# Kernel tuning notes

Hardware: AMD Instinct MI355X
Metric: run time of the kernel (lower is better)

## Reference

```python
import jax, jax.numpy as jnp
import numpy as np

INP_DIM = 1024
PROJ_DIM = 1024
SEQ = 2048
BATCH = 4

def setup_inputs() -> dict:
    key = jax.random.key(0)
    k1, k2, k3, k4 = jax.random.split(key, 4)
    inputs = jax.random.normal(k1, (BATCH, SEQ, INP_DIM), dtype=jnp.float32)
    # nn.Linear weights stored as (out, in); we keep them that way and transpose in matmul
    Wq = jax.random.normal(k2, (PROJ_DIM, INP_DIM), dtype=jnp.float32) * (1.0 / np.sqrt(INP_DIM))
    Wk = jax.random.normal(k3, (PROJ_DIM, INP_DIM), dtype=jnp.float32) * (1.0 / np.sqrt(INP_DIM))
    Wv = jax.random.normal(k4, (PROJ_DIM, INP_DIM), dtype=jnp.float32) * (1.0 / np.sqrt(INP_DIM))
    return {"inputs": inputs, "Wq": Wq, "Wk": Wk, "Wv": Wv}

def reference(inputs, Wq, Wk, Wv):
    # QKV projections: x @ W.T (nn.Linear convention)
    Q = jnp.einsum('bsd,pd->bsp', inputs, Wq)
    K = jnp.einsum('bsd,pd->bsp', inputs, Wk)
    V = jnp.einsum('bsd,pd->bsp', inputs, Wv)
    scores = jnp.einsum('bqp,bkp->bqk', Q, K)  # [B, S, S]
    n = inputs.shape[1]
    causal = jnp.tril(jnp.ones((n, n), dtype=bool))  # True = keep
    scores = jnp.where(causal, scores, -jnp.inf)
    weights = jax.nn.softmax(scores / jnp.sqrt(jnp.float32(Q.shape[-1])), axis=-1)
    # dropout rate = 0.0 -> identity
    Z = jnp.einsum('bqk,bkp->bqp', weights, V)
    return Z
```

## Files before the change

kernel.cpp:

```cpp
#include <hip/hip_runtime.h>
#include <stdint.h>

#define SEQ   2048
#define DIM   1024
#define BATCH 4

typedef _Float16 f16;
typedef __attribute__((ext_vector_type(8))) _Float16 f16x8;
typedef __attribute__((ext_vector_type(4))) _Float16 f16x4;
typedef __attribute__((ext_vector_type(4))) float   f32x4;

typedef void __attribute__((address_space(1))) vg_t;
typedef void __attribute__((address_space(3))) vl_t;

__device__ __forceinline__ void gld16(const void* g, void* l) {
  __builtin_amdgcn_global_load_lds((vg_t*)g, (vl_t*)l, 16, 0, 0);
}

__global__ __launch_bounds__(256) void cvt_all(const float* __restrict__ x,
                                               const float* __restrict__ wq,
                                               const float* __restrict__ wk,
                                               const float* __restrict__ wv,
                                               f16* __restrict__ xb,
                                               f16* __restrict__ wh) {
  const int bx = blockIdx.x;
  const float* in; f16* out; int base;
  if (bx < 8192)       { in = x;  out = xb;             base = bx; }
  else if (bx < 9216)  { in = wq; out = wh;             base = bx - 8192; }
  else if (bx < 10240) { in = wk; out = wh + (1 << 20); base = bx - 9216; }
  else                 { in = wv; out = wh + (2 << 20); base = bx - 10240; }
  const long i = ((long)base * 256 + threadIdx.x) * 4;
  float4 v = *(const float4*)(in + i);
  f16x4 o = { (f16)v.x, (f16)v.y, (f16)v.z, (f16)v.w };
  *(f16x4*)(out + i) = o;
}

template <int MODE, int CAUSAL, int BK>
__global__ __launch_bounds__(256) void gemm_bt(const f16* __restrict__ A, int lda, long aOffZ,
                                               const f16* __restrict__ B, int ldb, long bOffZ,
                                               void* __restrict__ Cv, int ldc, long cOffZ,
                                               int K) {
  constexpr int CH  = BK / 8;
  constexpr int RPL = 64 / CH;
  constexpr int NL  = 32 / RPL;
  __shared__ __align__(16) f16 lA[128 * BK];
  __shared__ __align__(16) f16 lB[128 * BK];

  const int tid  = threadIdx.x;
  const int wave = tid >> 6;
  const int lane = tid & 63;
  const int m0 = blockIdx.x * 128;
  const int n0 = blockIdx.y * 128;
  const int z  = blockIdx.z;

  if (CAUSAL == 1 && n0 >= m0 + 128) return;
  const int Keff = (CAUSAL == 2) ? (m0 + 128) : K;

  const f16* Ab = A + (long)z * aOffZ + (long)m0 * lda;
  const f16* Bb = B + (long)z * bOffZ + (long)n0 * ldb;

  const int wm = (wave & 1) * 64;
  const int wn = (wave >> 1) * 64;

  f32x4 acc[4][4] = {};

  const int srow = lane / CH;
  const int sj   = lane % CH;
  const int fr   = lane & 15;
  const int fq   = lane >> 4;

  for (int kt = 0; kt < Keff; kt += BK) {
    __syncthreads();
#pragma unroll
    for (int j = 0; j < NL; ++j) {
      const int rgrp = j * 4 + wave;
      const int row  = rgrp * RPL + srow;
      const int gch  = sj ^ (row & (CH - 1));
      gld16(Ab + (long)row * lda + kt + gch * 8, (void*)(lA + rgrp * 512 + lane * 8));
      gld16(Bb + (long)row * ldb + kt + gch * 8, (void*)(lB + rgrp * 512 + lane * 8));
    }
    __syncthreads();

#pragma unroll
    for (int kk = 0; kk < BK; kk += 32) {
      f16x8 af[4], bf[4];
#pragma unroll
      for (int i = 0; i < 4; ++i) {
        const int arow = wm + i * 16 + fr;
        const int ach  = (kk / 8 + fq) ^ (arow & (CH - 1));
        af[i] = *(const f16x8*)(lA + arow * BK + ach * 8);
        const int brow = wn + i * 16 + fr;
        const int bch  = (kk / 8 + fq) ^ (brow & (CH - 1));
        bf[i] = *(const f16x8*)(lB + brow * BK + bch * 8);
      }
#pragma unroll
      for (int mi = 0; mi < 4; ++mi)
#pragma unroll
        for (int ni = 0; ni < 4; ++ni)
          acc[mi][ni] = __builtin_amdgcn_mfma_f32_16x16x32_f16(af[mi], bf[ni], acc[mi][ni], 0, 0, 0);
    }
  }

#pragma unroll
  for (int mi = 0; mi < 4; ++mi) {
    const int row = m0 + wm + mi * 16 + fq * 4;
#pragma unroll
    for (int ni = 0; ni < 4; ++ni) {
      const int col = n0 + wn + ni * 16 + fr;
      if constexpr (MODE == 0) {
        float* C = (float*)Cv + (long)z * cOffZ;
#pragma unroll
        for (int r = 0; r < 4; ++r) C[(long)(row + r) * ldc + col] = acc[mi][ni][r];
      } else if constexpr (MODE == 1) {
        f16* C = (f16*)Cv + (long)z * cOffZ;
#pragma unroll
        for (int r = 0; r < 4; ++r) C[(long)(row + r) * ldc + col] = (f16)acc[mi][ni][r];
      } else if constexpr (MODE == 2) {
        f16* C = (f16*)Cv + (long)z * cOffZ;
        f16x4 o = { (f16)acc[mi][ni][0], (f16)acc[mi][ni][1],
                    (f16)acc[mi][ni][2], (f16)acc[mi][ni][3] };
        *(f16x4*)(C + (long)col * ldc + row) = o;
      } else {
        f16* Qh  = (f16*)Cv;
        f16* Kh  = Qh + (size_t)8 * 1024 * 1024;
        f16* VTb = Kh + (size_t)8 * 1024 * 1024;
        if (col < 1024) {
#pragma unroll
          for (int r = 0; r < 4; ++r) Qh[(long)(row + r) * DIM + col] = (f16)acc[mi][ni][r];
        } else if (col < 2048) {
#pragma unroll
          for (int r = 0; r < 4; ++r) Kh[(long)(row + r) * DIM + (col - 1024)] = (f16)acc[mi][ni][r];
        } else {
          f16x4 o = { (f16)acc[mi][ni][0], (f16)acc[mi][ni][1],
                      (f16)acc[mi][ni][2], (f16)acc[mi][ni][3] };
          *(f16x4*)(VTb + (long)(col - 2048) * (BATCH * SEQ) + row) = o;
        }
      }
    }
  }
}

__global__ __launch_bounds__(256) void softmax_causal(f16* S) {
  const int q = blockIdx.x, b = blockIdx.y;
  f16* row = S + ((long)b * SEQ + q) * SEQ;
  const int tid = threadIdx.x;
  const int lane = tid & 63, wave = tid >> 6;
  const int nvalid = q + 1;

  f16x8 vv = *(const f16x8*)(row + tid * 8);
  float v[8];
  float m = -3.0e38f;
#pragma unroll
  for (int i = 0; i < 8; ++i) {
    const int k = tid * 8 + i;
    v[i] = (k < nvalid) ? (float)vv[i] * 0.03125f : -3.0e38f;
    m = fmaxf(m, v[i]);
  }
#pragma unroll
  for (int off = 32; off; off >>= 1) m = fmaxf(m, __shfl_xor(m, off));
  __shared__ float redm[4], reds[4];
  if (lane == 0) redm[wave] = m;
  __syncthreads();
  m = fmaxf(fmaxf(redm[0], redm[1]), fmaxf(redm[2], redm[3]));

  float s = 0.f;
#pragma unroll
  for (int i = 0; i < 8; ++i) {
    const float p = (v[i] > -1.0e37f) ? __expf(v[i] - m) : 0.f;
    v[i] = p;
    s += p;
  }
#pragma unroll
  for (int off = 32; off; off >>= 1) s += __shfl_xor(s, off);
  if (lane == 0) reds[wave] = s;
  __syncthreads();
  s = reds[0] + reds[1] + reds[2] + reds[3];
  const float inv = 1.f / s;
  f16x8 o;
#pragma unroll
  for (int i = 0; i < 8; ++i) o[i] = (f16)(v[i] * inv);
  *(f16x8*)(row + tid * 8) = o;
}

extern "C" void kernel_launch(void* const* d_in, const int* in_sizes, int n_in,
                              void* d_out, int out_size, void* d_ws, size_t ws_size,
                              hipStream_t stream) {
  const float* x  = (const float*)d_in[0];
  const float* Wq = (const float*)d_in[1];
  const float* Wk = (const float*)d_in[2];
  const float* Wv = (const float*)d_in[3];
  float* out = (float*)d_out;

  if (ws_size < (size_t)51 * 1024 * 1024 * 2) return;

  f16* xb = (f16*)d_ws;
  f16* Wh = xb + (size_t)8 * 1024 * 1024;
  f16* Qh = Wh + (size_t)3 * 1024 * 1024;
  f16* Kh = Qh + (size_t)8 * 1024 * 1024;
  f16* VT = Kh + (size_t)8 * 1024 * 1024;
  f16* Sc = VT + (size_t)8 * 1024 * 1024;

  const long QOFF = (long)SEQ * DIM;
  const long SOFF = (long)SEQ * SEQ;

  cvt_all<<<11264, 256, 0, stream>>>(x, Wq, Wk, Wv, xb, Wh);

  gemm_bt<3, 0, 64><<<dim3(64, 24, 1), 256, 0, stream>>>(xb, DIM, 0, Wh, DIM, 0, Qh, 0, 0, DIM);

  gemm_bt<1, 1, 128><<<dim3(16, 16, 4), 256, 0, stream>>>(Qh, DIM, QOFF, Kh, DIM, QOFF,
                                                          Sc, SEQ, SOFF, DIM);

  softmax_causal<<<dim3(SEQ, BATCH), 256, 0, stream>>>(Sc);

  gemm_bt<0, 2, 128><<<dim3(16, 8, 4), 256, 0, stream>>>(Sc, SEQ, SOFF,
                                                         VT, BATCH * SEQ, SEQ,
                                                         out, DIM, (long)SEQ * DIM, SEQ);
}
```

Before: 244.4 us.

## Double-buffer LDS tiles in GEMM to overlap global loads with MFMA

Replaces the single-buffered shared-memory K loop with a two-stage ping-pong buffer so the next K tile's async global-to-LDS loads are issued before computing the current tile. BK is fixed at 64 for all GEMMs, so the two GEMMs that used BK=128 now run more, smaller iterations. LDS use per block stays at 64 KB. The goal is to hide global memory latency behind MFMA work, at the cost of fewer K elements per barrier interval for those GEMMs.

New measurement: 255.0 us. 1.04x slower.

```diff
diff --git a/kernel.cpp b/kernel.cpp
--- a/kernel.cpp
+++ b/kernel.cpp
@@ -35,16 +35,14 @@
   *(f16x4*)(out + i) = o;
 }
 
-template <int MODE, int CAUSAL, int BK>
+template <int MODE, int CAUSAL>
 __global__ __launch_bounds__(256) void gemm_bt(const f16* __restrict__ A, int lda, long aOffZ,
                                                const f16* __restrict__ B, int ldb, long bOffZ,
                                                void* __restrict__ Cv, int ldc, long cOffZ,
                                                int K) {
-  constexpr int CH  = BK / 8;
-  constexpr int RPL = 64 / CH;
-  constexpr int NL  = 32 / RPL;
-  __shared__ __align__(16) f16 lA[128 * BK];
-  __shared__ __align__(16) f16 lB[128 * BK];
+  constexpr int BK = 64;
+  __shared__ __align__(16) f16 lA[2][128 * BK];
+  __shared__ __align__(16) f16 lB[2][128 * BK];
 
   const int tid  = threadIdx.x;
   const int wave = tid >> 6;
@@ -64,40 +62,52 @@
 
   f32x4 acc[4][4] = {};
 
-  const int srow = lane / CH;
-  const int sj   = lane % CH;
+  const int srow = lane >> 3;
+  const int sj   = lane & 7;
   const int fr   = lane & 15;
   const int fq   = lane >> 4;
 
-  for (int kt = 0; kt < Keff; kt += BK) {
-    __syncthreads();
-#pragma unroll
-    for (int j = 0; j < NL; ++j) {
+  auto stage = [&](int buf, int kt) {
+#pragma unroll
+    for (int j = 0; j < 4; ++j) {
       const int rgrp = j * 4 + wave;
-      const int row  = rgrp * RPL + srow;
-      const int gch  = sj ^ (row & (CH - 1));
-      gld16(Ab + (long)row * lda + kt + gch * 8, (void*)(lA + rgrp * 512 + lane * 8));
-      gld16(Bb + (long)row * ldb + kt + gch * 8, (void*)(lB + rgrp * 512 + lane * 8));
-    }
-    __syncthreads();
-
+      const int row  = rgrp * 8 + srow;
+      const int gch  = sj ^ (row & 7);
+      gld16(Ab + (long)row * lda + kt + gch * 8, (void*)(&lA[buf][rgrp * 512 + lane * 8]));
+      gld16(Bb + (long)row * ldb + kt + gch * 8, (void*)(&lB[buf][rgrp * 512 + lane * 8]));
+    }
+  };
+
+  auto compute = [&](int buf) {
 #pragma unroll
     for (int kk = 0; kk < BK; kk += 32) {
       f16x8 af[4], bf[4];
 #pragma unroll
       for (int i = 0; i < 4; ++i) {
         const int arow = wm + i * 16 + fr;
-        const int ach  = (kk / 8 + fq) ^ (arow & (CH - 1));
-        af[i] = *(const f16x8*)(lA + arow * BK + ach * 8);
+        const int ach  = (kk / 8 + fq) ^ (arow & 7);
+        af[i] = *(const f16x8*)(&lA[buf][arow * BK + ach * 8]);
         const int brow = wn + i * 16 + fr;
-        const int bch  = (kk / 8 + fq) ^ (brow & (CH - 1));
-        bf[i] = *(const f16x8*)(lB + brow * BK + bch * 8);
+        const int bch  = (kk / 8 + fq) ^ (brow & 7);
+        bf[i] = *(const f16x8*)(&lB[buf][brow * BK + bch * 8]);
       }
 #pragma unroll
       for (int mi = 0; mi < 4; ++mi)
 #pragma unroll
         for (int ni = 0; ni < 4; ++ni)
           acc[mi][ni] = __builtin_amdgcn_mfma_f32_16x16x32_f16(af[mi], bf[ni], acc[mi][ni], 0, 0, 0);
+    }
+  };
+
+  stage(0, 0);
+  for (int kt = 0; kt < Keff; kt += 2 * BK) {
+    __syncthreads();
+    if (kt + BK < Keff) stage(1, kt + BK);
+    compute(0);
+    if (kt + BK < Keff) {
+      __syncthreads();
+      if (kt + 2 * BK < Keff) stage(0, kt + 2 * BK);
+      compute(1);
     }
   }
 
@@ -205,14 +215,14 @@
 
   cvt_all<<<11264, 256, 0, stream>>>(x, Wq, Wk, Wv, xb, Wh);
 
-  gemm_bt<3, 0, 64><<<dim3(64, 24, 1), 256, 0, stream>>>(xb, DIM, 0, Wh, DIM, 0, Qh, 0, 0, DIM);
-
-  gemm_bt<1, 1, 128><<<dim3(16, 16, 4), 256, 0, stream>>>(Qh, DIM, QOFF, Kh, DIM, QOFF,
-                                                          Sc, SEQ, SOFF, DIM);
+  gemm_bt<3, 0><<<dim3(64, 24, 1), 256, 0, stream>>>(xb, DIM, 0, Wh, DIM, 0, Qh, 0, 0, DIM);
+
+  gemm_bt<1, 1><<<dim3(16, 16, 4), 256, 0, stream>>>(Qh, DIM, QOFF, Kh, DIM, QOFF,
+                                                     Sc, SEQ, SOFF, DIM);
 
   softmax_causal<<<dim3(SEQ, BATCH), 256, 0, stream>>>(Sc);
 
-  gemm_bt<0, 2, 128><<<dim3(16, 8, 4), 256, 0, stream>>>(Sc, SEQ, SOFF,
-                                                         VT, BATCH * SEQ, SEQ,
-                                                         out, DIM, (long)SEQ * DIM, SEQ);
-}
+  gemm_bt<0, 2><<<dim3(16, 8, 4), 256, 0, stream>>>(Sc, SEQ, SOFF,
+                                                    VT, BATCH * SEQ, SEQ,
+                                                    out, DIM, (long)SEQ * DIM, SEQ);
+}
```
